# Optimization experiments

Measured on AMD Instinct MI355X. Metric: run time of the kernel, lower is better.

The kernel has to match this reference:

```python
import jax, jax.numpy as jnp
import numpy as np

N = 50000       # nodes
E = 800000      # edges
IN = 128        # in_channels
H = 8           # heads
C = 32          # out_channels per head
HC = H * C      # 256
NEG_SLOPE = 0.2


def setup_inputs() -> dict:
    key = jax.random.key(0)
    ks = jax.random.split(key, 8)
    s_in = 1.0 / np.sqrt(IN)
    s_c = 1.0 / np.sqrt(C)
    x = jax.random.normal(ks[0], (N, IN), dtype=jnp.float32)
    edge_index = jax.random.randint(ks[1], (2, E), 0, N, dtype=jnp.int64)
    W_l = jax.random.normal(ks[2], (IN, HC), dtype=jnp.float32) * s_in   # lin_l weight
    W_r = jax.random.normal(ks[3], (IN, HC), dtype=jnp.float32) * s_in   # lin_r weight
    att = jax.random.normal(ks[4], (H, C), dtype=jnp.float32) * s_c      # attention vector a
    bias = jax.random.normal(ks[5], (HC,), dtype=jnp.float32) * 0.02
    Wp = jax.random.normal(ks[6], (IN, HC), dtype=jnp.float32) * s_in    # residual proj weight
    bp = jax.random.normal(ks[7], (HC,), dtype=jnp.float32) * 0.02
    return {"x": x, "edge_index": edge_index, "W_l": W_l, "W_r": W_r,
            "att": att, "bias": bias, "Wp": Wp, "bp": bp}


def _gatv2_forward(x, edge_index, W_l, W_r, att, bias, Wp, bp):
    src = edge_index[0]  # source j (message sender)
    dst = edge_index[1]  # target i (softmax segment)
    xl = (x @ W_l).reshape(N, H, C)  # messages / left branch
    xr = (x @ W_r).reshape(N, H, C)  # right (target) branch
    # per-edge GATv2 score: a^T LeakyReLU(xl_j + xr_i)
    e = xl[src] + xr[dst]                              # [E, H, C]
    e = jnp.where(e >= 0, e, NEG_SLOPE * e)            # LeakyReLU(0.2)
    score = jnp.einsum('ehc,hc->eh', e, att)           # [E, H]
    # segment softmax over incoming edges of each target node
    m = jax.ops.segment_max(score, dst, num_segments=N)   # [N, H]
    m = jnp.where(jnp.isfinite(m), m, 0.0)                 # empty segments -> 0
    ex = jnp.exp(score - m[dst])                            # [E, H]
    denom = jax.ops.segment_sum(ex, dst, num_segments=N)   # [N, H]
    alpha = ex / jnp.maximum(denom[dst], 1e-16)             # [E, H]
    # scatter-aggregate alpha-weighted source messages
    msg = alpha[:, :, None] * xl[src]                       # [E, H, C]
    out = jax.ops.segment_sum(msg, dst, num_segments=N)    # [N, H, C]
    out = out.reshape(N, HC) + bias
    # residual projection + GELU (exact erf, like torch F.gelu default)
    res = x @ Wp + bp
    return jax.nn.gelu(out + res, approximate=False)


def reference(x, edge_index, W_l, W_r, att, bias, Wp, bp):
    return _gatv2_forward(x, edge_index, W_l, W_r, att, bias, Wp, bp)
```

## Files before the change

### kernel.cpp

```cpp
#include <hip/hip_runtime.h>
#include <math.h>

#define N_NODES 50000
#define N_EDGES 800000
#define K_IN    128
#define HC      256
#define NCOLS   768

typedef __bf16 bf16x8 __attribute__((ext_vector_type(8)));
typedef float  f32x4  __attribute__((ext_vector_type(4)));

__device__ inline ushort f32_to_bf16(float f)
{
    union { float f; uint u; } c; c.f = f;
    uint r = c.u + 0x7fff + ((c.u >> 16) & 1);
    return (ushort)(r >> 16);
}
__device__ inline float bf16_to_f32(ushort u)
{
    union { uint u; float f; } c; c.u = (uint)u << 16;
    return c.f;
}
__device__ inline float4 bf4_to_f4(uint2 u)
{
    float4 r;
    r.x = __uint_as_float(u.x << 16);
    r.y = __uint_as_float(u.x & 0xffff0000u);
    r.z = __uint_as_float(u.y << 16);
    r.w = __uint_as_float(u.y & 0xffff0000u);
    return r;
}

__global__ void convert_x_kernel(const float* __restrict__ x,
                                 ushort* __restrict__ Xh, ushort* __restrict__ Xl)
{
    int t = blockIdx.x * 256 + threadIdx.x;
    if (t >= N_NODES * (K_IN / 4)) return;
    float4 v = reinterpret_cast<const float4*>(x)[t];
    ushort h0 = f32_to_bf16(v.x), h1 = f32_to_bf16(v.y);
    ushort h2 = f32_to_bf16(v.z), h3 = f32_to_bf16(v.w);
    ushort l0 = f32_to_bf16(v.x - bf16_to_f32(h0));
    ushort l1 = f32_to_bf16(v.y - bf16_to_f32(h1));
    ushort l2 = f32_to_bf16(v.z - bf16_to_f32(h2));
    ushort l3 = f32_to_bf16(v.w - bf16_to_f32(h3));
    reinterpret_cast<uint2*>(Xh)[t] =
        make_uint2((uint)h0 | ((uint)h1 << 16), (uint)h2 | ((uint)h3 << 16));
    reinterpret_cast<uint2*>(Xl)[t] =
        make_uint2((uint)l0 | ((uint)l1 << 16), (uint)l2 | ((uint)l3 << 16));
}

__global__ void convert_w_kernel(const float* __restrict__ Wl,
                                 const float* __restrict__ Wr,
                                 const float* __restrict__ Wp,
                                 ushort* __restrict__ Wt_hi,
                                 ushort* __restrict__ Wt_lo)
{
    int t = blockIdx.x * 256 + threadIdx.x;
    if (t >= NCOLS * K_IN) return;
    int n = t >> 7, k = t & 127;
    const float* W = (n < 256) ? Wl : (n < 512) ? Wr : Wp;
    int nn = n & 255;
    float v = W[(size_t)k * HC + nn];
    ushort h = f32_to_bf16(v);
    Wt_hi[t] = h;
    Wt_lo[t] = f32_to_bf16(v - bf16_to_f32(h));
}

__global__ __launch_bounds__(256, 2) void gemm_mfma_kernel(
    const ushort* __restrict__ Xh, const ushort* __restrict__ Xl,
    const ushort* __restrict__ Wt_hi, const ushort* __restrict__ Wt_lo,
    const float* __restrict__ bp,
    ushort* __restrict__ xfb, float* __restrict__ res)
{
    __shared__ ushort Ah[128 * 64], Al[128 * 64], Bh[128 * 64], Bl[128 * 64];

    const int bm = blockIdx.x;
    const int bn = blockIdx.y;
    const int nbase = bn * 128;
    const int tid = threadIdx.x;
    const int lane = tid & 63;
    const int w = tid >> 6;
    const int wr = w >> 1, wc = w & 1;
    const int fr = lane & 15;
    const int kg = lane >> 4;

    f32x4 acc[4][4];
#pragma unroll
    for (int mi = 0; mi < 4; ++mi)
#pragma unroll
        for (int ni = 0; ni < 4; ++ni) acc[mi][ni] = (f32x4)0.f;

#pragma unroll
    for (int ks = 0; ks < 2; ++ks) {
        const int k0 = ks * 64;
#pragma unroll
        for (int i = 0; i < 8; ++i) {
            int f = tid + i * 256;
            int r = f >> 4, q = f & 15;
            int grow = bm * 128 + r;
            uint2 hv = make_uint2(0u, 0u), lv = make_uint2(0u, 0u);
            if (grow < N_NODES) {
                size_t g = (size_t)grow * K_IN + k0 + q * 4;
                hv = *reinterpret_cast<const uint2*>(&Xh[g]);
                lv = *reinterpret_cast<const uint2*>(&Xl[g]);
            }
            int off = r * 64 + ((q * 4) ^ ((r & 7) << 3));
            *reinterpret_cast<uint2*>(&Ah[off]) = hv;
            *reinterpret_cast<uint2*>(&Al[off]) = lv;
        }
#pragma unroll
        for (int i = 0; i < 8; ++i) {
            int f = tid + i * 256;
            int n = f >> 4, q = f & 15;
            size_t g = (size_t)(nbase + n) * K_IN + k0 + q * 4;
            uint2 hv = *reinterpret_cast<const uint2*>(&Wt_hi[g]);
            uint2 lv = *reinterpret_cast<const uint2*>(&Wt_lo[g]);
            int off = n * 64 + ((q * 4) ^ ((n & 7) << 3));
            *reinterpret_cast<uint2*>(&Bh[off]) = hv;
            *reinterpret_cast<uint2*>(&Bl[off]) = lv;
        }
        __syncthreads();
#pragma unroll
        for (int kk = 0; kk < 2; ++kk) {
            const int kush = kk * 32 + kg * 8;
            bf16x8 ah[4], al[4], bh[4], blo[4];
#pragma unroll
            for (int mi = 0; mi < 4; ++mi) {
                int row = wr * 64 + mi * 16 + fr;
                int off = row * 64 + (kush ^ ((row & 7) << 3));
                ah[mi] = *reinterpret_cast<const bf16x8*>(&Ah[off]);
                al[mi] = *reinterpret_cast<const bf16x8*>(&Al[off]);
            }
#pragma unroll
            for (int ni = 0; ni < 4; ++ni) {
                int nrow = wc * 64 + ni * 16 + fr;
                int off = nrow * 64 + (kush ^ ((nrow & 7) << 3));
                bh[ni]  = *reinterpret_cast<const bf16x8*>(&Bh[off]);
                blo[ni] = *reinterpret_cast<const bf16x8*>(&Bl[off]);
            }
#pragma unroll
            for (int mi = 0; mi < 4; ++mi)
#pragma unroll
                for (int ni = 0; ni < 4; ++ni) {
                    acc[mi][ni] = __builtin_amdgcn_mfma_f32_16x16x32_bf16(ah[mi], bh[ni],  acc[mi][ni], 0, 0, 0);
                    acc[mi][ni] = __builtin_amdgcn_mfma_f32_16x16x32_bf16(al[mi], bh[ni],  acc[mi][ni], 0, 0, 0);
                    acc[mi][ni] = __builtin_amdgcn_mfma_f32_16x16x32_bf16(ah[mi], blo[ni], acc[mi][ni], 0, 0, 0);
                }
        }
        __syncthreads();
    }

    if (bn < 4) {
#pragma unroll
        for (int mi = 0; mi < 4; ++mi)
#pragma unroll
            for (int i = 0; i < 4; ++i) {
                int row = bm * 128 + wr * 64 + mi * 16 + kg * 4 + i;
                if (row >= N_NODES) continue;
#pragma unroll
                for (int ni = 0; ni < 4; ++ni) {
                    int col = nbase + wc * 64 + ni * 16 + fr;
                    xfb[(size_t)row * 512 + col] = f32_to_bf16(acc[mi][ni][i]);
                }
            }
    } else {
        float badd[4];
#pragma unroll
        for (int ni = 0; ni < 4; ++ni)
            badd[ni] = bp[nbase - 512 + wc * 64 + ni * 16 + fr];
#pragma unroll
        for (int mi = 0; mi < 4; ++mi)
#pragma unroll
            for (int i = 0; i < 4; ++i) {
                int row = bm * 128 + wr * 64 + mi * 16 + kg * 4 + i;
                if (row >= N_NODES) continue;
#pragma unroll
                for (int ni = 0; ni < 4; ++ni) {
                    int col = nbase - 512 + wc * 64 + ni * 16 + fr;
                    res[(size_t)row * 256 + col] = acc[mi][ni][i] + badd[ni];
                }
            }
    }
}

#define SCAN_CH 1024
#define SCAN_NB ((N_NODES + SCAN_CH - 1) / SCAN_CH)

__global__ void zero_int_kernel(int* __restrict__ p, int n)
{
    int i = blockIdx.x * blockDim.x + threadIdx.x;
    if (i < n) p[i] = 0;
}

__global__ void hist_kernel(const int* __restrict__ ei, int* __restrict__ deg)
{
    int e = blockIdx.x * blockDim.x + threadIdx.x;
    if (e < N_EDGES) atomicAdd(&deg[ei[N_EDGES + e]], 1);
}

__device__ inline int wave_incl_scan(int v, int lane)
{
#pragma unroll
    for (int off = 1; off < 64; off <<= 1) {
        int t = __shfl_up(v, off, 64);
        if (lane >= off) v += t;
    }
    return v;
}

__device__ inline int wave_sum(int v)
{
#pragma unroll
    for (int off = 1; off < 64; off <<= 1) v += __shfl_xor(v, off, 64);
    return v;
}

__global__ __launch_bounds__(1024) void scan_partial_kernel(
    const int* __restrict__ deg, int* __restrict__ bsum)
{
    __shared__ int wsum[16];
    int i = blockIdx.x * SCAN_CH + threadIdx.x;
    int lane = threadIdx.x & 63, wid = threadIdx.x >> 6;
    int v = (i < N_NODES) ? deg[i] : 0;
    int s = wave_sum(v);
    if (lane == 0) wsum[wid] = s;
    __syncthreads();
    if (threadIdx.x == 0) {
        int t = 0;
#pragma unroll
        for (int k = 0; k < 16; ++k) t += wsum[k];
        bsum[blockIdx.x] = t;
    }
}

__global__ void scan_base_kernel(const int* __restrict__ bsum,
                                 int* __restrict__ bbase, int* __restrict__ offs)
{
    int lane = threadIdx.x;
    int v = (lane < SCAN_NB) ? bsum[lane] : 0;
    int inc = wave_incl_scan(v, lane);
    if (lane < SCAN_NB) bbase[lane] = inc - v;
    if (lane == 63) offs[N_NODES] = inc;
}

__global__ __launch_bounds__(1024) void scan_final_kernel(
    const int* __restrict__ deg, const int* __restrict__ bbase,
    int* __restrict__ offs, int* __restrict__ cursor)
{
    __shared__ int wsum[16];
    int i = blockIdx.x * SCAN_CH + threadIdx.x;
    int lane = threadIdx.x & 63, wid = threadIdx.x >> 6;
    int v = (i < N_NODES) ? deg[i] : 0;
    int inc = wave_incl_scan(v, lane);
    if (lane == 63) wsum[wid] = inc;
    __syncthreads();
    if (wid == 0) {
        int wv = (lane < 16) ? wsum[lane] : 0;
        int ws = wave_incl_scan(wv, lane);
        if (lane < 16) wsum[lane] = ws;
    }
    __syncthreads();
    int wbase = wid ? wsum[wid - 1] : 0;
    int excl = bbase[blockIdx.x] + wbase + inc - v;
    if (i < N_NODES) { offs[i] = excl; cursor[i] = excl; }
}

__global__ void scatter_kernel(const int* __restrict__ ei,
                               int* __restrict__ cursor, int* __restrict__ csr)
{
    int e = blockIdx.x * blockDim.x + threadIdx.x;
    if (e < N_EDGES) {
        int s = ei[e];
        int d = ei[N_EDGES + e];
        int pos = atomicAdd(&cursor[d], 1);
        csr[pos] = s;
    }
}

__device__ inline float escore(float4 v, float4 xrv, float4 a1, float4 a2)
{
    float x0 = v.x + xrv.x, x1 = v.y + xrv.y, x2 = v.z + xrv.z, x3 = v.w + xrv.w;
    float p = a1.x * x0 + a2.x * fabsf(x0);
    p = fmaf(a1.y, x1, p); p = fmaf(a2.y, fabsf(x1), p);
    p = fmaf(a1.z, x2, p); p = fmaf(a2.z, fabsf(x2), p);
    p = fmaf(a1.w, x3, p); p = fmaf(a2.w, fabsf(x3), p);
    p += __shfl_xor(p, 1, 64);
    p += __shfl_xor(p, 2, 64);
    p += __shfl_xor(p, 4, 64);
    return p;
}

__global__ __launch_bounds__(256) void gat_agg_kernel(
    const ushort* __restrict__ xfb, const float* __restrict__ res,
    const int* __restrict__ offs, const int* __restrict__ csr,
    const float* __restrict__ att, const float* __restrict__ bias,
    float* __restrict__ out)
{
    const int lane = threadIdx.x & 63;
    const int wid = threadIdx.x >> 6;
    const int node = blockIdx.x * 4 + wid;
    if (node >= N_NODES) return;

    const uint2* __restrict__ xfb2 = reinterpret_cast<const uint2*>(xfb);
    const float4 attv = reinterpret_cast<const float4*>(att)[lane];
    float4 a1, a2;
    a1.x = 0.6f * attv.x; a1.y = 0.6f * attv.y; a1.z = 0.6f * attv.z; a1.w = 0.6f * attv.w;
    a2.x = 0.4f * attv.x; a2.y = 0.4f * attv.y; a2.z = 0.4f * attv.z; a2.w = 0.4f * attv.w;
    const float4 xrv = bf4_to_f4(xfb2[(uint)node * 128u + 64u + lane]);

    const int e0 = offs[node];
    const int e1 = offs[node + 1];

    float m = 0.f, d = 0.f;
    float4 acc = make_float4(0.f, 0.f, 0.f, 0.f);

    int e = e0;
    if (e < e1) {
        int s = csr[e];
        float4 v = bf4_to_f4(xfb2[((uint)s << 7) + lane]);
        m = escore(v, xrv, a1, a2);
        d = 1.f;
        acc = v;
        ++e;
    }
    for (; e + 3 < e1; e += 4) {
        int s0 = csr[e], s1 = csr[e + 1], s2 = csr[e + 2], s3 = csr[e + 3];
        float4 v0 = bf4_to_f4(xfb2[((uint)s0 << 7) + lane]);
        float4 v1 = bf4_to_f4(xfb2[((uint)s1 << 7) + lane]);
        float4 v2 = bf4_to_f4(xfb2[((uint)s2 << 7) + lane]);
        float4 v3 = bf4_to_f4(xfb2[((uint)s3 << 7) + lane]);
        float p0 = escore(v0, xrv, a1, a2);
        float p1 = escore(v1, xrv, a1, a2);
        float p2 = escore(v2, xrv, a1, a2);
        float p3 = escore(v3, xrv, a1, a2);
        float w0 = __expf(p0 - m), w1 = __expf(p1 - m);
        float w2 = __expf(p2 - m), w3 = __expf(p3 - m);
        d += (w0 + w1) + (w2 + w3);
        acc.x = fmaf(w3, v3.x, fmaf(w2, v2.x, fmaf(w1, v1.x, fmaf(w0, v0.x, acc.x))));
        acc.y = fmaf(w3, v3.y, fmaf(w2, v2.y, fmaf(w1, v1.y, fmaf(w0, v0.y, acc.y))));
        acc.z = fmaf(w3, v3.z, fmaf(w2, v2.z, fmaf(w1, v1.z, fmaf(w0, v0.z, acc.z))));
        acc.w = fmaf(w3, v3.w, fmaf(w2, v2.w, fmaf(w1, v1.w, fmaf(w0, v0.w, acc.w))));
    }
    for (; e < e1; ++e) {
        int s0 = csr[e];
        float4 v0 = bf4_to_f4(xfb2[((uint)s0 << 7) + lane]);
        float p0 = escore(v0, xrv, a1, a2);
        float w0 = __expf(p0 - m);
        d += w0;
        acc.x = fmaf(w0, v0.x, acc.x);
        acc.y = fmaf(w0, v0.y, acc.y);
        acc.z = fmaf(w0, v0.z, acc.z);
        acc.w = fmaf(w0, v0.w, acc.w);
    }

    float inv = 1.f / fmaxf(d, 1e-16f);
    const float4 bv = reinterpret_cast<const float4*>(bias)[lane];
    const float4 rv = reinterpret_cast<const float4*>(res)[(uint)node * 64u + lane];
    float4 o;
    o.x = acc.x * inv + bv.x + rv.x;
    o.y = acc.y * inv + bv.y + rv.y;
    o.z = acc.z * inv + bv.z + rv.z;
    o.w = acc.w * inv + bv.w + rv.w;
    o.x = 0.5f * o.x * (1.f + erff(o.x * 0.70710678118654752f));
    o.y = 0.5f * o.y * (1.f + erff(o.y * 0.70710678118654752f));
    o.z = 0.5f * o.z * (1.f + erff(o.z * 0.70710678118654752f));
    o.w = 0.5f * o.w * (1.f + erff(o.w * 0.70710678118654752f));
    reinterpret_cast<float4*>(out)[(uint)node * 64u + lane] = o;
}

extern "C" void kernel_launch(void* const* d_in, const int* in_sizes, int n_in,
                              void* d_out, int out_size, void* d_ws, size_t ws_size,
                              hipStream_t stream)
{
    const float* x    = (const float*)d_in[0];
    const int*   ei   = (const int*)d_in[1];
    const float* Wl   = (const float*)d_in[2];
    const float* Wr   = (const float*)d_in[3];
    const float* att  = (const float*)d_in[4];
    const float* bias = (const float*)d_in[5];
    const float* Wp   = (const float*)d_in[6];
    const float* bp   = (const float*)d_in[7];
    float* out = (float*)d_out;

    ushort* xfb   = (ushort*)d_ws;
    float*  res   = (float*)(xfb + (size_t)N_NODES * 512);
    ushort* Xh    = (ushort*)(res + (size_t)N_NODES * 256);
    ushort* Xl    = Xh + (size_t)N_NODES * K_IN;
    ushort* Wt_hi = Xl + (size_t)N_NODES * K_IN;
    ushort* Wt_lo = Wt_hi + NCOLS * K_IN;
    int* deg    = (int*)(Wt_lo + NCOLS * K_IN);
    int* offs   = deg + N_NODES;
    int* cursor = offs + N_NODES + 1;
    int* csr    = cursor + N_NODES;
    int* bsum   = csr + N_EDGES;
    int* bbase  = bsum + SCAN_NB;

    hipLaunchKernelGGL(convert_x_kernel, dim3((N_NODES * (K_IN / 4) + 255) / 256), dim3(256), 0, stream,
                       x, Xh, Xl);
    hipLaunchKernelGGL(convert_w_kernel, dim3((NCOLS * K_IN + 255) / 256), dim3(256), 0, stream,
                       Wl, Wr, Wp, Wt_hi, Wt_lo);
    hipLaunchKernelGGL(zero_int_kernel, dim3((N_NODES + 255) / 256), dim3(256), 0, stream,
                       deg, N_NODES);
    hipLaunchKernelGGL(hist_kernel, dim3((N_EDGES + 255) / 256), dim3(256), 0, stream,
                       ei, deg);
    hipLaunchKernelGGL(scan_partial_kernel, dim3(SCAN_NB), dim3(1024), 0, stream,
                       deg, bsum);
    hipLaunchKernelGGL(scan_base_kernel, dim3(1), dim3(64), 0, stream,
                       bsum, bbase, offs);
    hipLaunchKernelGGL(scan_final_kernel, dim3(SCAN_NB), dim3(1024), 0, stream,
                       deg, bbase, offs, cursor);
    hipLaunchKernelGGL(scatter_kernel, dim3((N_EDGES + 255) / 256), dim3(256), 0, stream,
                       ei, cursor, csr);
    hipLaunchKernelGGL(gemm_mfma_kernel, dim3((N_NODES + 127) / 128, 6), dim3(256), 0, stream,
                       Xh, Xl, Wt_hi, Wt_lo, bp, xfb, res);
    hipLaunchKernelGGL(gat_agg_kernel, dim3((N_NODES + 3) / 4), dim3(256), 0, stream,
                       xfb, res, offs, csr, att, bias, out);
}
```

Before: 325.7 us.

## Split wave into two half-waves processing alternate edges with 16-byte loads and DPP reductions

```diff
diff --git a/kernel.cpp b/kernel.cpp
--- a/kernel.cpp
+++ b/kernel.cpp
@@ -21,14 +21,16 @@
     union { uint u; float f; } c; c.u = (uint)u << 16;
     return c.f;
 }
-__device__ inline float4 bf4_to_f4(uint2 u)
-{
-    float4 r;
-    r.x = __uint_as_float(u.x << 16);
-    r.y = __uint_as_float(u.x & 0xffff0000u);
-    r.z = __uint_as_float(u.y << 16);
-    r.w = __uint_as_float(u.y & 0xffff0000u);
-    return r;
+__device__ inline void bf8_to_f8(uint4 u, float* f)
+{
+    f[0] = __uint_as_float(u.x << 16);
+    f[1] = __uint_as_float(u.x & 0xffff0000u);
+    f[2] = __uint_as_float(u.y << 16);
+    f[3] = __uint_as_float(u.y & 0xffff0000u);
+    f[4] = __uint_as_float(u.z << 16);
+    f[5] = __uint_as_float(u.z & 0xffff0000u);
+    f[6] = __uint_as_float(u.w << 16);
+    f[7] = __uint_as_float(u.w & 0xffff0000u);
 }
 
 __global__ void convert_x_kernel(const float* __restrict__ x,
@@ -277,16 +279,29 @@
     }
 }
 
-__device__ inline float escore(float4 v, float4 xrv, float4 a1, float4 a2)
-{
-    float x0 = v.x + xrv.x, x1 = v.y + xrv.y, x2 = v.z + xrv.z, x3 = v.w + xrv.w;
-    float p = a1.x * x0 + a2.x * fabsf(x0);
-    p = fmaf(a1.y, x1, p); p = fmaf(a2.y, fabsf(x1), p);
-    p = fmaf(a1.z, x2, p); p = fmaf(a2.z, fabsf(x2), p);
-    p = fmaf(a1.w, x3, p); p = fmaf(a2.w, fabsf(x3), p);
-    p += __shfl_xor(p, 1, 64);
-    p += __shfl_xor(p, 2, 64);
-    p += __shfl_xor(p, 4, 64);
+__device__ inline float dpp_add_xor1(float p)
+{
+    int q = __builtin_amdgcn_update_dpp(0, __float_as_int(p), 0xB1, 0xF, 0xF, true);
+    return p + __int_as_float(q);
+}
+__device__ inline float dpp_add_xor2(float p)
+{
+    int q = __builtin_amdgcn_update_dpp(0, __float_as_int(p), 0x4E, 0xF, 0xF, true);
+    return p + __int_as_float(q);
+}
+
+__device__ inline float score8(const float* v, const float* xr8,
+                               const float* a1, const float* a2)
+{
+    float p = 0.f;
+#pragma unroll
+    for (int i = 0; i < 8; ++i) {
+        float t = v[i] + xr8[i];
+        p = fmaf(a1[i], t, p);
+        p = fmaf(a2[i], fabsf(t), p);
+    }
+    p = dpp_add_xor1(p);
+    p = dpp_add_xor2(p);
     return p;
 }
 
@@ -301,71 +316,85 @@
     const int node = blockIdx.x * 4 + wid;
     if (node >= N_NODES) return;
 
-    const uint2* __restrict__ xfb2 = reinterpret_cast<const uint2*>(xfb);
-    const float4 attv = reinterpret_cast<const float4*>(att)[lane];
-    float4 a1, a2;
-    a1.x = 0.6f * attv.x; a1.y = 0.6f * attv.y; a1.z = 0.6f * attv.z; a1.w = 0.6f * attv.w;
-    a2.x = 0.4f * attv.x; a2.y = 0.4f * attv.y; a2.z = 0.4f * attv.z; a2.w = 0.4f * attv.w;
-    const float4 xrv = bf4_to_f4(xfb2[(uint)node * 128u + 64u + lane]);
+    const int c8 = lane & 31;
+    const int half = lane >> 5;
+
+    float a1[8], a2[8], xr8[8];
+    {
+        float4 t0 = reinterpret_cast<const float4*>(att)[c8 * 2];
+        float4 t1 = reinterpret_cast<const float4*>(att)[c8 * 2 + 1];
+        float av[8] = {t0.x, t0.y, t0.z, t0.w, t1.x, t1.y, t1.z, t1.w};
+#pragma unroll
+        for (int i = 0; i < 8; ++i) { a1[i] = 0.6f * av[i]; a2[i] = 0.4f * av[i]; }
+    }
+    {
+        uint4 u = *reinterpret_cast<const uint4*>(&xfb[(uint)node * 512u + 256u + (uint)c8 * 8u]);
+        bf8_to_f8(u, xr8);
+    }
 
     const int e0 = offs[node];
     const int e1 = offs[node + 1];
 
     float m = 0.f, d = 0.f;
-    float4 acc = make_float4(0.f, 0.f, 0.f, 0.f);
+    float acc[8] = {0.f, 0.f, 0.f, 0.f, 0.f, 0.f, 0.f, 0.f};
 
     int e = e0;
     if (e < e1) {
         int s = csr[e];
-        float4 v = bf4_to_f4(xfb2[((uint)s << 7) + lane]);
-        m = escore(v, xrv, a1, a2);
-        d = 1.f;
-        acc = v;
+        uint4 u = *reinterpret_cast<const uint4*>(&xfb[(uint)s * 512u + (uint)c8 * 8u]);
+        float v[8]; bf8_to_f8(u, v);
+        m = score8(v, xr8, a1, a2);
+        float w0 = (half == 0) ? 1.f : 0.f;
+        d = w0;
+#pragma unroll
+        for (int i = 0; i < 8; ++i) acc[i] = v[i] * w0;
         ++e;
     }
-    for (; e + 3 < e1; e += 4) {
-        int s0 = csr[e], s1 = csr[e + 1], s2 = csr[e + 2], s3 = csr[e + 3];
-        float4 v0 = bf4_to_f4(xfb2[((uint)s0 << 7) + lane]);
-        float4 v1 = bf4_to_f4(xfb2[((uint)s1 << 7) + lane]);
-        float4 v2 = bf4_to_f4(xfb2[((uint)s2 << 7) + lane]);
-        float4 v3 = bf4_to_f4(xfb2[((uint)s3 << 7) + lane]);
-        float p0 = escore(v0, xrv, a1, a2);
-        float p1 = escore(v1, xrv, a1, a2);
-        float p2 = escore(v2, xrv, a1, a2);
-        float p3 = escore(v3, xrv, a1, a2);
-        float w0 = __expf(p0 - m), w1 = __expf(p1 - m);
-        float w2 = __expf(p2 - m), w3 = __expf(p3 - m);
-        d += (w0 + w1) + (w2 + w3);
-        acc.x = fmaf(w3, v3.x, fmaf(w2, v2.x, fmaf(w1, v1.x, fmaf(w0, v0.x, acc.x))));
-        acc.y = fmaf(w3, v3.y, fmaf(w2, v2.y, fmaf(w1, v1.y, fmaf(w0, v0.y, acc.y))));
-        acc.z = fmaf(w3, v3.z, fmaf(w2, v2.z, fmaf(w1, v1.z, fmaf(w0, v0.z, acc.z))));
-        acc.w = fmaf(w3, v3.w, fmaf(w2, v2.w, fmaf(w1, v1.w, fmaf(w0, v0.w, acc.w))));
-    }
-    for (; e < e1; ++e) {
-        int s0 = csr[e];
-        float4 v0 = bf4_to_f4(xfb2[((uint)s0 << 7) + lane]);
-        float p0 = escore(v0, xrv, a1, a2);
-        float w0 = __expf(p0 - m);
-        d += w0;
-        acc.x = fmaf(w0, v0.x, acc.x);
-        acc.y = fmaf(w0, v0.y, acc.y);
-        acc.z = fmaf(w0, v0.z, acc.z);
-        acc.w = fmaf(w0, v0.w, acc.w);
-    }
-
-    float inv = 1.f / fmaxf(d, 1e-16f);
-    const float4 bv = reinterpret_cast<const float4*>(bias)[lane];
-    const float4 rv = reinterpret_cast<const float4*>(res)[(uint)node * 64u + lane];
-    float4 o;
-    o.x = acc.x * inv + bv.x + rv.x;
-    o.y = acc.y * inv + bv.y + rv.y;
-    o.z = acc.z * inv + bv.z + rv.z;
-    o.w = acc.w * inv + bv.w + rv.w;
-    o.x = 0.5f * o.x * (1.f + erff(o.x * 0.70710678118654752f));
-    o.y = 0.5f * o.y * (1.f + erff(o.y * 0.70710678118654752f));
-    o.z = 0.5f * o.z * (1.f + erff(o.z * 0.70710678118654752f));
-    o.w = 0.5f * o.w * (1.f + erff(o.w * 0.70710678118654752f));
-    reinterpret_cast<float4*>(out)[(uint)node * 64u + lane] = o;
+    for (; e + 1 < e1; e += 2) {
+        int sA = csr[e], sB = csr[e + 1];
+        int s = half ? sB : sA;
+        uint4 u = *reinterpret_cast<const uint4*>(&xfb[(uint)s * 512u + (uint)c8 * 8u]);
+        float v[8]; bf8_to_f8(u, v);
+        float p = score8(v, xr8, a1, a2);
+        float w = __expf(p - m);
+        d += w;
+#pragma unroll
+        for (int i = 0; i < 8; ++i) acc[i] = fmaf(w, v[i], acc[i]);
+    }
+    if (e < e1) {
+        int s = csr[e];
+        uint4 u = *reinterpret_cast<const uint4*>(&xfb[(uint)s * 512u + (uint)c8 * 8u]);
+        float v[8]; bf8_to_f8(u, v);
+        float p = score8(v, xr8, a1, a2);
+        float w = (half == 0) ? __expf(p - m) : 0.f;
+        d += w;
+#pragma unroll
+        for (int i = 0; i < 8; ++i) acc[i] = fmaf(w, v[i], acc[i]);
+    }
+
+    d += __shfl_xor(d, 32, 64);
+#pragma unroll
+    for (int i = 0; i < 8; ++i) acc[i] += __shfl_xor(acc[i], 32, 64);
+
+    if (half == 0) {
+        float inv = 1.f / fmaxf(d, 1e-16f);
+        float4 b0 = reinterpret_cast<const float4*>(bias)[c8 * 2];
+        float4 b1 = reinterpret_cast<const float4*>(bias)[c8 * 2 + 1];
+        float4 r0 = reinterpret_cast<const float4*>(res)[(uint)node * 64u + c8 * 2];
+        float4 r1 = reinterpret_cast<const float4*>(res)[(uint)node * 64u + c8 * 2 + 1];
+        float bv[8] = {b0.x, b0.y, b0.z, b0.w, b1.x, b1.y, b1.z, b1.w};
+        float rv[8] = {r0.x, r0.y, r0.z, r0.w, r1.x, r1.y, r1.z, r1.w};
+        float o[8];
+#pragma unroll
+        for (int i = 0; i < 8; ++i) {
+            float t = fmaf(acc[i], inv, bv[i] + rv[i]);
+            o[i] = 0.5f * t * (1.f + erff(t * 0.70710678118654752f));
+        }
+        float4 o0 = make_float4(o[0], o[1], o[2], o[3]);
+        float4 o1 = make_float4(o[4], o[5], o[6], o[7]);
+        reinterpret_cast<float4*>(out)[(uint)node * 64u + c8 * 2] = o0;
+        reinterpret_cast<float4*>(out)[(uint)node * 64u + c8 * 2 + 1] = o1;
+    }
 }
 
 extern "C" void kernel_launch(void* const* d_in, const int* in_sizes, int n_in,
```

Measured after the change: 338.6 us. +4.0%, slower.
